# Optimization experiments

Hardware: AMD Instinct MI355X
Metric: run time of the kernel (lower is better)

## Reference

```python
import jax, jax.numpy as jnp
import numpy as np

N_NODES = 100000
N_EDGES = 1600000
UNITS = 256
N_LAYERS = 4          # model_layers
NUM_GRAPHS = 512
IN_FEAT = 9


def _glorot(key, shape):
    lim = float(np.sqrt(6.0 / (shape[0] + shape[1])))
    return jax.random.uniform(key, shape, jnp.float32, -lim, lim)


def setup_inputs() -> dict:
    key = jax.random.key(0)
    ks = jax.random.split(key, 16)
    x = jax.random.normal(ks[0], (N_NODES, IN_FEAT), jnp.float32)
    edge_index = jax.random.randint(ks[1], (2, N_EDGES), 0, N_NODES, jnp.int64)
    batch = jnp.sort(jax.random.randint(ks[2], (N_NODES,), 0, NUM_GRAPHS, jnp.int64))
    Win = _glorot(ks[3], (IN_FEAT, UNITS))
    bin_ = jnp.zeros((UNITS,), jnp.float32)
    Ws = jnp.stack([_glorot(ks[4 + i], (UNITS, UNITS)) for i in range(N_LAYERS - 1)])
    bs = jnp.zeros((N_LAYERS - 1, UNITS), jnp.float32)
    fc1_w = _glorot(ks[8], (UNITS, UNITS))
    fc1_b = jnp.zeros((UNITS,), jnp.float32)
    fc2_w = _glorot(ks[9], (UNITS, 32))
    fc2_b = jnp.zeros((32,), jnp.float32)
    fc3_w = _glorot(ks[10], (32, 1))
    fc3_b = jnp.zeros((1,), jnp.float32)
    return dict(x=x, edge_index=edge_index, batch=batch, Win=Win, bin_=bin_,
                Ws=Ws, bs=bs, fc1_w=fc1_w, fc1_b=fc1_b, fc2_w=fc2_w,
                fc2_b=fc2_b, fc3_w=fc3_w, fc3_b=fc3_b)


def _gcn_conv(x, W, b, src, dst, dinv):
    # PyG GCNConv: h = xW ; out = D^-1/2 (A+I) D^-1/2 h + b  (self-loops added)
    h = x @ W                                     # [N, d]
    norm = dinv[src] * dinv[dst]                  # [E]
    agg = jnp.zeros_like(h).at[dst].add(h[src] * norm[:, None])
    agg = agg + h * (dinv * dinv)[:, None]        # self-loop term
    return agg + b


def reference(x, edge_index, batch, Win, bin_, Ws, bs,
              fc1_w, fc1_b, fc2_w, fc2_b, fc3_w, fc3_b):
    src, dst = edge_index[0], edge_index[1]
    # degree with self-loops
    deg = jnp.zeros((N_NODES,), jnp.float32).at[dst].add(1.0) + 1.0
    dinv = jax.lax.rsqrt(deg)

    h = jnp.tanh(_gcn_conv(x, Win, bin_, src, dst, dinv))
    for i in range(N_LAYERS - 1):
        h = jnp.tanh(_gcn_conv(h, Ws[i], bs[i], src, dst, dinv))
        # dropout: identity at inference
    h = jnp.tanh(h @ fc1_w + fc1_b)
    h = jnp.tanh(h @ fc2_w + fc2_b)
    h = h @ fc3_w + fc3_b                          # [N, 1]
    # global mean pool over graphs
    sums = jax.ops.segment_sum(h, batch, num_segments=NUM_GRAPHS)      # [G, 1]
    cnts = jax.ops.segment_sum(jnp.ones((N_NODES,), jnp.float32), batch,
                               num_segments=NUM_GRAPHS)
    pooled = sums / jnp.maximum(cnts, 1.0)[:, None]
    return jax.nn.sigmoid(pooled)
```

## Files before the change

kernel.cpp:

```cpp
#include <hip/hip_runtime.h>
#include <math.h>

#define N_NODES 100000
#define N_EDGES 1600000
#define UNITS   256
#define NGRAPH  512
#define IN_FEAT 9
#define NB_SCAN ((N_NODES + 255) / 256)
#define NBUK    ((N_NODES + 255) / 256)
#define BCAP    8192
#define EPB     16384
#define NPB     ((N_EDGES + EPB - 1) / EPB)

typedef short bf16x8 __attribute__((ext_vector_type(8)));
typedef float f32x4  __attribute__((ext_vector_type(4)));
typedef float f32x2  __attribute__((ext_vector_type(2)));

__device__ __forceinline__ float bflo(unsigned int u) {
  return __builtin_bit_cast(float, u << 16);
}
__device__ __forceinline__ float bfhi(unsigned int u) {
  return __builtin_bit_cast(float, u & 0xffff0000u);
}
__device__ __forceinline__ unsigned short f2bf(float f) {
  unsigned int u = __builtin_bit_cast(unsigned int, f);
  u += 0x7fffu + ((u >> 16) & 1u);
  return (unsigned short)(u >> 16);
}

__device__ __forceinline__ bf16x8 f8tobf(uint2 q) {
  f32x2 v0 = __builtin_amdgcn_cvt_pk_f32_fp8(q.x, false);
  f32x2 v1 = __builtin_amdgcn_cvt_pk_f32_fp8(q.x, true);
  f32x2 v2 = __builtin_amdgcn_cvt_pk_f32_fp8(q.y, false);
  f32x2 v3 = __builtin_amdgcn_cvt_pk_f32_fp8(q.y, true);
  bf16x8 a;
  a[0] = (short)f2bf(v0[0]); a[1] = (short)f2bf(v0[1]);
  a[2] = (short)f2bf(v1[0]); a[3] = (short)f2bf(v1[1]);
  a[4] = (short)f2bf(v2[0]); a[5] = (short)f2bf(v2[1]);
  a[6] = (short)f2bf(v3[0]); a[7] = (short)f2bf(v3[1]);
  return a;
}

__device__ __forceinline__ int swz(int row, int byteInRow) {
  return row * 128 + (byteInRow ^ ((row & 7) << 4));
}


__global__ __launch_bounds__(256) void k_part(const int* __restrict__ ei,
                                              int* __restrict__ bcnt,
                                              uint2* __restrict__ bstore) {
  __shared__ int hist[NBUK];
  __shared__ int base[NBUK];
  int tid = threadIdx.x;
  int e0 = blockIdx.x * EPB;
  for (int i = tid; i < NBUK; i += 256) hist[i] = 0;
  __syncthreads();
  #pragma unroll 4
  for (int j = 0; j < EPB / 256; ++j) {
    int e = e0 + j * 256 + tid;
    if (e < N_EDGES) atomicAdd(&hist[ei[N_EDGES + e] >> 8], 1);
  }
  __syncthreads();
  for (int i = tid; i < NBUK; i += 256) {
    int h = hist[i];
    base[i] = h ? atomicAdd(&bcnt[i], h) : 0;
    hist[i] = 0;
  }
  __syncthreads();
  #pragma unroll 4
  for (int j = 0; j < EPB / 256; ++j) {
    int e = e0 + j * 256 + tid;
    if (e < N_EDGES) {
      int s = ei[e];
      int d = ei[N_EDGES + e];
      int b = d >> 8;
      int pos = base[b] + atomicAdd(&hist[b], 1);
      bstore[(size_t)b * BCAP + pos] = make_uint2((unsigned)s, (unsigned)d);
    }
  }
}

__global__ __launch_bounds__(256) void k_cnt(const int* __restrict__ bcnt,
                                             const uint2* __restrict__ bstore,
                                             int* __restrict__ cnt) {
  __shared__ int h[256];
  int b = blockIdx.x, tid = threadIdx.x;
  h[tid] = 0;
  __syncthreads();
  int nE = bcnt[b];
  for (int i = tid; i < nE; i += 256)
    atomicAdd(&h[bstore[(size_t)b * BCAP + i].y & 255], 1);
  __syncthreads();
  int node = b * 256 + tid;
  if (node < N_NODES) cnt[node] = h[tid];
}

__global__ __launch_bounds__(256) void k_colfill(const int* __restrict__ bcnt,
                                                 const uint2* __restrict__ bstore,
                                                 const int* __restrict__ row_ptr,
                                                 int* __restrict__ col) {
  __shared__ int cur[256];
  int b = blockIdx.x, tid = threadIdx.x;
  int node = b * 256 + tid;
  cur[tid] = (node < N_NODES) ? row_ptr[node] : 0;
  __syncthreads();
  int nE = bcnt[b];
  for (int i = tid; i < nE; i += 256) {
    uint2 sd = bstore[(size_t)b * BCAP + i];
    int pos = atomicAdd(&cur[sd.y & 255], 1);
    col[pos] = (int)sd.x;
  }
}

__global__ __launch_bounds__(256) void k_bsum(const int* __restrict__ cnt,
                                              int* __restrict__ bsum) {
  __shared__ int wsS[4];
  int b = blockIdx.x, tid = threadIdx.x, lane = tid & 63, w = tid >> 6;
  int idx = b * 256 + tid;
  int s = (idx < N_NODES) ? cnt[idx] : 0;
  #pragma unroll
  for (int m = 32; m >= 1; m >>= 1) s += __shfl_xor(s, m);
  if (lane == 0) wsS[w] = s;
  __syncthreads();
  if (tid == 0) bsum[b] = wsS[0] + wsS[1] + wsS[2] + wsS[3];
}

__global__ __launch_bounds__(512) void k_bscan(int* __restrict__ bsum) {
  __shared__ int wsS[8];
  int tid = threadIdx.x, lane = tid & 63, w = tid >> 6;
  int v = (tid < NB_SCAN) ? bsum[tid] : 0;
  int s = v;
  #pragma unroll
  for (int off = 1; off < 64; off <<= 1) {
    int t = __shfl_up(s, off);
    if (lane >= off) s += t;
  }
  if (lane == 63) wsS[w] = s;
  __syncthreads();
  int woff = 0;
  #pragma unroll
  for (int i = 0; i < 8; ++i) woff += (i < w) ? wsS[i] : 0;
  if (tid < NB_SCAN) bsum[tid] = woff + s - v;
}

__global__ __launch_bounds__(256) void k_scan3(const int* __restrict__ cnt,
                                               const int* __restrict__ bsum,
                                               int* __restrict__ row_ptr) {
  __shared__ int wsS[4];
  int b = blockIdx.x, tid = threadIdx.x, lane = tid & 63, w = tid >> 6;
  int idx = b * 256 + tid;
  int v = (idx < N_NODES) ? cnt[idx] : 0;
  int s = v;
  #pragma unroll
  for (int off = 1; off < 64; off <<= 1) {
    int t = __shfl_up(s, off);
    if (lane >= off) s += t;
  }
  if (lane == 63) wsS[w] = s;
  __syncthreads();
  int woff = 0;
  #pragma unroll
  for (int i = 0; i < 4; ++i) woff += (i < w) ? wsS[i] : 0;
  if (idx < N_NODES) row_ptr[idx] = bsum[b] + woff + s - v;
  if (idx == 0) row_ptr[N_NODES] = N_EDGES;
}

__global__ void k_dinv(const int* __restrict__ cnt, float* __restrict__ dinv) {
  int n = blockIdx.x * blockDim.x + threadIdx.x;
  if (n < N_NODES) dinv[n] = rsqrtf((float)cnt[n] + 1.0f);
}

__global__ void k_bounds(const int* __restrict__ batch, int* __restrict__ starts) {
  int g = blockIdx.x * blockDim.x + threadIdx.x;
  if (g > NGRAPH) return;
  if (g == NGRAPH) { starts[g] = N_NODES; return; }
  int lo = 0, hi = N_NODES;
  while (lo < hi) { int m = (lo + hi) >> 1; if (batch[m] < g) lo = m + 1; else hi = m; }
  starts[g] = lo;
}


__global__ void k_cvtW(const float* __restrict__ Ws, const float* __restrict__ fc1_w,
                       unsigned short* __restrict__ Wt) {
  int idx = blockIdx.x * 256 + threadIdx.x;
  int m = idx >> 16;
  int r = idx & 65535;
  int n = r >> 8;
  int k = r & 255;
  const float* src = (m < 3) ? (Ws + (size_t)m * 65536) : fc1_w;
  Wt[idx] = f2bf(src[k * 256 + n]);
}

__global__ void k_cvtW2(const float* __restrict__ fc2_w, unsigned short* __restrict__ Wt2) {
  int idx = blockIdx.x * 256 + threadIdx.x;
  int n = idx >> 8;
  int k = idx & 255;
  Wt2[idx] = f2bf(fc2_w[k * 32 + n]);
}

__global__ void k_scalex(const float* __restrict__ x, const float* __restrict__ dinv,
                         float* __restrict__ xs) {
  int idx = blockIdx.x * blockDim.x + threadIdx.x;
  if (idx < N_NODES * IN_FEAT) xs[idx] = x[idx] * dinv[idx / IN_FEAT];
}


__global__ void k_agg9(const float* __restrict__ xs, const int* __restrict__ row_ptr,
                       const int* __restrict__ col, const float* __restrict__ dinv,
                       float* __restrict__ p0) {
  int n = blockIdx.x * blockDim.x + threadIdx.x;
  if (n >= N_NODES) return;
  float acc[IN_FEAT];
  #pragma unroll
  for (int j = 0; j < IN_FEAT; ++j) acc[j] = xs[n * IN_FEAT + j];
  int beg = row_ptr[n], end = row_ptr[n + 1];
  for (int e = beg; e < end; ++e) {
    int s = col[e];
    #pragma unroll
    for (int j = 0; j < IN_FEAT; ++j) acc[j] += xs[s * IN_FEAT + j];
  }
  float dn = dinv[n];
  #pragma unroll
  for (int j = 0; j < IN_FEAT; ++j) p0[n * IN_FEAT + j] = dn * acc[j];
}

__global__ __launch_bounds__(256) void k_gemm9(const float* __restrict__ p0,
                                               const float* __restrict__ Win,
                                               const float* __restrict__ bin,
                                               const float* __restrict__ scale,
                                               unsigned char* __restrict__ h8) {
  __shared__ float pS[32][IN_FEAT];
  int tid = threadIdx.x;
  int row0 = blockIdx.x * 32;
  for (int i = tid; i < 32 * IN_FEAT; i += 256) {
    int r = i / IN_FEAT;
    pS[r][i % IN_FEAT] = (row0 + r < N_NODES) ? p0[(size_t)row0 * IN_FEAT + i] : 0.0f;
  }
  float wcol[IN_FEAT];
  #pragma unroll
  for (int k = 0; k < IN_FEAT; ++k) wcol[k] = Win[k * UNITS + tid];
  float b = bin[tid];
  __syncthreads();
  for (int r = 0; r < 32; ++r) {
    int gr = row0 + r;
    if (gr >= N_NODES) break;
    float a = b;
    #pragma unroll
    for (int k = 0; k < IN_FEAT; ++k) a += pS[r][k] * wcol[k];
    float v = scale[gr] * tanhf(a);
    float vn = __shfl_xor(v, 1);
    if ((tid & 1) == 0) {
      unsigned int pk = __builtin_amdgcn_cvt_pk_fp8_f32(v, vn, 0, false);
      *(unsigned short*)(h8 + (size_t)gr * UNITS + tid) = (unsigned short)pk;
    }
  }
}


__global__ __launch_bounds__(256) void k_agg256(
    const unsigned int* __restrict__ hs8,
    const int* __restrict__ row_ptr, const int* __restrict__ col,
    const float* __restrict__ dinv, unsigned int* __restrict__ p8) {
  int wid = threadIdx.x >> 6;
  int lane = threadIdx.x & 63;
  int n = blockIdx.x * 4 + wid;
  if (n >= N_NODES) return;
  unsigned int q = hs8[(size_t)n * 64 + lane];
  f32x2 lo = __builtin_amdgcn_cvt_pk_f32_fp8(q, false);
  f32x2 hi = __builtin_amdgcn_cvt_pk_f32_fp8(q, true);
  float a0 = lo[0], a1 = lo[1], a2 = hi[0], a3 = hi[1];
  int e = row_ptr[n], end = row_ptr[n + 1];
  for (; e + 8 <= end; e += 8) {
    int s[8];
    unsigned int qq[8];
    #pragma unroll
    for (int j = 0; j < 8; ++j) s[j] = col[e + j];
    #pragma unroll
    for (int j = 0; j < 8; ++j) qq[j] = hs8[(size_t)s[j] * 64 + lane];
    #pragma unroll
    for (int j = 0; j < 8; ++j) {
      f32x2 l2 = __builtin_amdgcn_cvt_pk_f32_fp8(qq[j], false);
      f32x2 h2 = __builtin_amdgcn_cvt_pk_f32_fp8(qq[j], true);
      a0 += l2[0]; a1 += l2[1]; a2 += h2[0]; a3 += h2[1];
    }
  }
  if (e + 4 <= end) {
    int s[4];
    unsigned int qq[4];
    #pragma unroll
    for (int j = 0; j < 4; ++j) s[j] = col[e + j];
    #pragma unroll
    for (int j = 0; j < 4; ++j) qq[j] = hs8[(size_t)s[j] * 64 + lane];
    #pragma unroll
    for (int j = 0; j < 4; ++j) {
      f32x2 l2 = __builtin_amdgcn_cvt_pk_f32_fp8(qq[j], false);
      f32x2 h2 = __builtin_amdgcn_cvt_pk_f32_fp8(qq[j], true);
      a0 += l2[0]; a1 += l2[1]; a2 += h2[0]; a3 += h2[1];
    }
    e += 4;
  }
  for (; e < end; ++e) {
    unsigned int q0 = hs8[(size_t)col[e] * 64 + lane];
    f32x2 l2 = __builtin_amdgcn_cvt_pk_f32_fp8(q0, false);
    f32x2 h2 = __builtin_amdgcn_cvt_pk_f32_fp8(q0, true);
    a0 += l2[0]; a1 += l2[1]; a2 += h2[0]; a3 += h2[1];
  }
  float dn = dinv[n];
  unsigned int u = __builtin_amdgcn_cvt_pk_fp8_f32(dn * a0, dn * a1, 0, false);
  u = __builtin_amdgcn_cvt_pk_fp8_f32(dn * a2, dn * a3, u, true);
  p8[(size_t)n * 64 + lane] = u;
}


__global__ __launch_bounds__(256, 4) void k_gemm_f8(
    const unsigned char* __restrict__ A8,
    const unsigned short* __restrict__ Wt,
    const float* __restrict__ bias,
    const float* __restrict__ scale,
    unsigned char* __restrict__ C8,
    int M) {
  __shared__ __align__(16) char lds[33792];
  char* Bs = lds;
  unsigned short (*Cs)[264] = (unsigned short(*)[264])lds;

  const int tid = threadIdx.x;
  const int w = tid >> 6;
  const int l = tid & 63;
  const int l15 = l & 15;
  const int blk = l >> 4;
  const int wr = w >> 1, wc = w & 1;
  const int row0 = blockIdx.x * 64;

  const int sr = tid >> 3;
  const int sc = (tid & 7) * 16;

  const unsigned char* aRow[2];
  #pragma unroll
  for (int rf = 0; rf < 2; ++rf) {
    int gr = row0 + 32 * wr + rf * 16 + l15;
    if (gr >= M) gr = M - 1;
    aRow[rf] = A8 + (size_t)gr * UNITS + 8 * blk;
  }

  f32x4 acc[2][8];
  #pragma unroll
  for (int rf = 0; rf < 2; ++rf)
    #pragma unroll
    for (int cf = 0; cf < 8; ++cf) acc[rf][cf] = (f32x4){0.f, 0.f, 0.f, 0.f};

  for (int ks = 0; ks < 4; ++ks) {
    const int k0 = ks * 64;
    if (ks) __syncthreads();
    #pragma unroll
    for (int i = 0; i < 8; ++i) {
      int n = sr + i * 32;
      uint4 v = *(const uint4*)(Wt + (size_t)n * UNITS + k0 + (sc >> 1));
      *(uint4*)(Bs + swz(n, sc)) = v;
    }
    __syncthreads();
    #pragma unroll
    for (int kc = 0; kc < 2; ++kc) {
      bf16x8 a[2];
      #pragma unroll
      for (int rf = 0; rf < 2; ++rf) {
        uint2 q = *(const uint2*)(aRow[rf] + k0 + kc * 32);
        a[rf] = f8tobf(q);
      }
      #pragma unroll
      for (int cf = 0; cf < 8; ++cf) {
        bf16x8 b = *(const bf16x8*)(Bs + swz(128 * wc + cf * 16 + l15, kc * 64 + blk * 16));
        acc[0][cf] = __builtin_amdgcn_mfma_f32_16x16x32_bf16(a[0], b, acc[0][cf], 0, 0, 0);
        acc[1][cf] = __builtin_amdgcn_mfma_f32_16x16x32_bf16(a[1], b, acc[1][cf], 0, 0, 0);
      }
    }
  }

  __syncthreads();
  float dvv[2][4];
  #pragma unroll
  for (int rf = 0; rf < 2; ++rf)
    #pragma unroll
    for (int reg = 0; reg < 4; ++reg) {
      int gr = row0 + 32 * wr + rf * 16 + 4 * blk + reg;
      dvv[rf][reg] = scale ? scale[gr < M ? gr : M - 1] : 1.0f;
    }
  #pragma unroll
  for (int cf = 0; cf < 8; ++cf) {
    float bcol = bias[128 * wc + cf * 16 + l15];
    #pragma unroll
    for (int rf = 0; rf < 2; ++rf) {
      #pragma unroll
      for (int reg = 0; reg < 4; ++reg) {
        float v = dvv[rf][reg] * tanhf(acc[rf][cf][reg] + bcol);
        Cs[32 * wr + rf * 16 + 4 * blk + reg][128 * wc + cf * 16 + l15] = f2bf(v);
      }
    }
  }
  __syncthreads();
  #pragma unroll
  for (int j = 0; j < 8; ++j) {
    int flat = tid + j * 256;
    int r = flat >> 5;
    int c = flat & 31;
    int gr = row0 + r;
    if (gr < M) {
      uint4 v = *(const uint4*)&Cs[r][c * 8];
      uint2 u;
      u.x = __builtin_amdgcn_cvt_pk_fp8_f32(bflo(v.x), bfhi(v.x), 0, false);
      u.x = __builtin_amdgcn_cvt_pk_fp8_f32(bflo(v.y), bfhi(v.y), u.x, true);
      u.y = __builtin_amdgcn_cvt_pk_fp8_f32(bflo(v.z), bfhi(v.z), 0, false);
      u.y = __builtin_amdgcn_cvt_pk_fp8_f32(bflo(v.w), bfhi(v.w), u.y, true);
      *(uint2*)(C8 + (size_t)gr * UNITS + c * 8) = u;
    }
  }
}


__global__ __launch_bounds__(256) void k_fc23(
    const unsigned char* __restrict__ H8,
    const unsigned short* __restrict__ Wt2,
    const float* __restrict__ b2,
    const float* __restrict__ w3, const float* __restrict__ b3,
    float* __restrict__ ns, int M) {
  const int tid = threadIdx.x;
  const int w = tid >> 6;
  const int l = tid & 63;
  const int l15 = l & 15;
  const int blk = l >> 4;
  const int row0 = blockIdx.x * 64 + 16 * w;

  int r = row0 + l15;
  int rc = r < M ? r : M - 1;
  const unsigned char* aPtr = H8 + (size_t)rc * UNITS + 8 * blk;
  const unsigned short* bPtr = Wt2 + (size_t)l15 * UNITS + 8 * blk;

  f32x4 acc0 = (f32x4){0.f, 0.f, 0.f, 0.f};
  f32x4 acc1 = (f32x4){0.f, 0.f, 0.f, 0.f};
  #pragma unroll
  for (int k0 = 0; k0 < UNITS; k0 += 32) {
    bf16x8 a  = f8tobf(*(const uint2*)(aPtr + k0));
    bf16x8 b0 = *(const bf16x8*)(bPtr + k0);
    bf16x8 b1 = *(const bf16x8*)(bPtr + 16 * UNITS + k0);
    acc0 = __builtin_amdgcn_mfma_f32_16x16x32_bf16(a, b0, acc0, 0, 0, 0);
    acc1 = __builtin_amdgcn_mfma_f32_16x16x32_bf16(a, b1, acc1, 0, 0, 0);
  }

  float c0 = b2[l15], c1 = b2[16 + l15];
  float w30 = w3[l15], w31 = w3[16 + l15];
  float b3v = b3[0];
  #pragma unroll
  for (int reg = 0; reg < 4; ++reg) {
    float part = tanhf(acc0[reg] + c0) * w30 + tanhf(acc1[reg] + c1) * w31;
    #pragma unroll
    for (int m = 8; m >= 1; m >>= 1) part += __shfl_xor(part, m);
    int gr = row0 + 4 * blk + reg;
    if (l15 == 0 && gr < M) ns[gr] = part + b3v;
  }
}

__global__ __launch_bounds__(64) void k_pool(const float* __restrict__ ns,
                                             const int* __restrict__ starts,
                                             float* __restrict__ out) {
  int g = blockIdx.x;
  int lane = threadIdx.x;
  int s = starts[g], e = starts[g + 1];
  float acc = 0.0f;
  for (int i = s + lane; i < e; i += 64) acc += ns[i];
  #pragma unroll
  for (int m = 32; m >= 1; m >>= 1) acc += __shfl_xor(acc, m);
  if (lane == 0) {
    float mean = acc / fmaxf((float)(e - s), 1.0f);
    out[g] = 1.0f / (1.0f + expf(-mean));
  }
}


extern "C" void kernel_launch(void* const* d_in, const int* in_sizes, int n_in,
                              void* d_out, int out_size, void* d_ws, size_t ws_size,
                              hipStream_t stream) {
  const float* x     = (const float*)d_in[0];
  const int*   ei    = (const int*)d_in[1];
  const int*   batch = (const int*)d_in[2];
  const float* Win   = (const float*)d_in[3];
  const float* bin_  = (const float*)d_in[4];
  const float* Ws    = (const float*)d_in[5];
  const float* bs    = (const float*)d_in[6];
  const float* fc1_w = (const float*)d_in[7];
  const float* fc1_b = (const float*)d_in[8];
  const float* fc2_w = (const float*)d_in[9];
  const float* fc2_b = (const float*)d_in[10];
  const float* fc3_w = (const float*)d_in[11];
  const float* fc3_b = (const float*)d_in[12];
  float* out = (float*)d_out;

  char* ws = (char*)d_ws;
  size_t off = 0;
  auto alloc = [&](size_t bytes) {
    size_t o = off;
    off = (off + bytes + 255) & ~(size_t)255;
    return o;
  };
  int*   cnt     = (int*)(ws + alloc(N_NODES * 4));
  int*   row_ptr = (int*)(ws + alloc((N_NODES + 1) * 4));
  float* dinv    = (float*)(ws + alloc(N_NODES * 4));
  int*   col     = (int*)(ws + alloc((size_t)N_EDGES * 4));
  int*   bsum    = (int*)(ws + alloc(NB_SCAN * 4));
  int*   bcnt    = (int*)(ws + alloc(NBUK * 4));
  uint2* bstore  = (uint2*)(ws + alloc((size_t)NBUK * BCAP * 8));
  int*   starts  = (int*)(ws + alloc((NGRAPH + 1) * 4));
  float* ns      = (float*)(ws + alloc(N_NODES * 4));
  float* xs      = (float*)(ws + alloc((size_t)N_NODES * IN_FEAT * 4));
  float* p0      = (float*)(ws + alloc((size_t)N_NODES * IN_FEAT * 4));
  unsigned short* Wt   = (unsigned short*)(ws + alloc((size_t)4 * UNITS * UNITS * 2));
  unsigned short* Wt2  = (unsigned short*)(ws + alloc((size_t)32 * UNITS * 2));
  unsigned char*  h8a  = (unsigned char*)(ws + alloc((size_t)N_NODES * UNITS));
  unsigned char*  h8b  = (unsigned char*)(ws + alloc((size_t)N_NODES * UNITS));
  unsigned char*  p8   = (unsigned char*)(ws + alloc((size_t)N_NODES * UNITS));

  hipMemsetAsync(bcnt, 0, NBUK * 4, stream);

  k_cvtW<<<(4 * UNITS * UNITS) / 256, 256, 0, stream>>>(Ws, fc1_w, Wt);
  k_cvtW2<<<32, 256, 0, stream>>>(fc2_w, Wt2);

  k_part<<<NPB, 256, 0, stream>>>(ei, bcnt, bstore);
  k_cnt<<<NBUK, 256, 0, stream>>>(bcnt, bstore, cnt);
  k_bsum<<<NB_SCAN, 256, 0, stream>>>(cnt, bsum);
  k_bscan<<<1, 512, 0, stream>>>(bsum);
  k_scan3<<<NB_SCAN, 256, 0, stream>>>(cnt, bsum, row_ptr);
  k_dinv<<<(N_NODES + 255) / 256, 256, 0, stream>>>(cnt, dinv);
  k_colfill<<<NBUK, 256, 0, stream>>>(bcnt, bstore, row_ptr, col);
  k_bounds<<<3, 256, 0, stream>>>(batch, starts);

  k_scalex<<<(N_NODES * IN_FEAT + 255) / 256, 256, 0, stream>>>(x, dinv, xs);
  k_agg9<<<(N_NODES + 255) / 256, 256, 0, stream>>>(xs, row_ptr, col, dinv, p0);
  k_gemm9<<<(N_NODES + 31) / 32, 256, 0, stream>>>(p0, Win, bin_, dinv, h8a);

  int ggrid = (N_NODES + 63) / 64;
  k_agg256<<<(N_NODES + 3) / 4, 256, 0, stream>>>((const unsigned int*)h8a, row_ptr, col, dinv, (unsigned int*)p8);
  k_gemm_f8<<<ggrid, 256, 0, stream>>>(p8, Wt + (size_t)0 * UNITS * UNITS,
                                       bs + (size_t)0 * UNITS, dinv, h8b, N_NODES);
  k_agg256<<<(N_NODES + 3) / 4, 256, 0, stream>>>((const unsigned int*)h8b, row_ptr, col, dinv, (unsigned int*)p8);
  k_gemm_f8<<<ggrid, 256, 0, stream>>>(p8, Wt + (size_t)1 * UNITS * UNITS,
                                       bs + (size_t)1 * UNITS, dinv, h8a, N_NODES);
  k_agg256<<<(N_NODES + 3) / 4, 256, 0, stream>>>((const unsigned int*)h8a, row_ptr, col, dinv, (unsigned int*)p8);
  k_gemm_f8<<<ggrid, 256, 0, stream>>>(p8, Wt + (size_t)2 * UNITS * UNITS,
                                       bs + (size_t)2 * UNITS, nullptr, h8b, N_NODES);

  k_gemm_f8<<<ggrid, 256, 0, stream>>>(h8b, Wt + (size_t)3 * UNITS * UNITS,
                                       fc1_b, nullptr, h8a, N_NODES);

  k_fc23<<<(N_NODES + 63) / 64, 256, 0, stream>>>(h8a, Wt2, fc2_b, fc3_w, fc3_b, ns, N_NODES);

  k_pool<<<NGRAPH, 64, 0, stream>>>(ns, starts, out);
}
```

Before: 533.8 us.

## Fuse last GCN GEMM, fc1 and fc2/fc3 into one MLP kernel keeping activations in LDS

Replaces the final k_gemm_f8 (layer 4), the fc1 k_gemm_f8 and k_fc23 with a single k_mlp kernel that keeps the 64x256 bf16 intermediate tile in LDS between the three matmuls. This avoids two round trips of a 100000x256 fp8 activation through global memory, along with the fp8 requantisation at each step. It also folds the dinv computation into the scan kernel and shrinks edges per block in the partition kernel. The fused kernel uses 64KB of LDS, which may limit occupancy.

```diff
diff --git a/kernel.cpp b/kernel.cpp
--- a/kernel.cpp
+++ b/kernel.cpp
@@ -9,7 +9,7 @@
 #define NB_SCAN ((N_NODES + 255) / 256)
 #define NBUK    ((N_NODES + 255) / 256)
 #define BCAP    8192
-#define EPB     16384
+#define EPB     4096
 #define NPB     ((N_EDGES + EPB - 1) / EPB)
 
 typedef short bf16x8 __attribute__((ext_vector_type(8)));
@@ -44,6 +44,9 @@
 __device__ __forceinline__ int swz(int row, int byteInRow) {
   return row * 128 + (byteInRow ^ ((row & 7) << 4));
 }
+__device__ __forceinline__ int swzA(int row, int byteInRow) {
+  return row * 512 + (byteInRow ^ ((row & 7) << 4));
+}
 
 
 __global__ __launch_bounds__(256) void k_part(const int* __restrict__ ei,
@@ -145,7 +148,8 @@
 
 __global__ __launch_bounds__(256) void k_scan3(const int* __restrict__ cnt,
                                                const int* __restrict__ bsum,
-                                               int* __restrict__ row_ptr) {
+                                               int* __restrict__ row_ptr,
+                                               float* __restrict__ dinv) {
   __shared__ int wsS[4];
   int b = blockIdx.x, tid = threadIdx.x, lane = tid & 63, w = tid >> 6;
   int idx = b * 256 + tid;
@@ -161,13 +165,11 @@
   int woff = 0;
   #pragma unroll
   for (int i = 0; i < 4; ++i) woff += (i < w) ? wsS[i] : 0;
-  if (idx < N_NODES) row_ptr[idx] = bsum[b] + woff + s - v;
+  if (idx < N_NODES) {
+    row_ptr[idx] = bsum[b] + woff + s - v;
+    dinv[idx] = rsqrtf((float)v + 1.0f);
+  }
   if (idx == 0) row_ptr[N_NODES] = N_EDGES;
-}
-
-__global__ void k_dinv(const int* __restrict__ cnt, float* __restrict__ dinv) {
-  int n = blockIdx.x * blockDim.x + threadIdx.x;
-  if (n < N_NODES) dinv[n] = rsqrtf((float)cnt[n] + 1.0f);
 }
 
 __global__ void k_bounds(const int* __restrict__ batch, int* __restrict__ starts) {
@@ -382,7 +384,7 @@
     #pragma unroll
     for (int reg = 0; reg < 4; ++reg) {
       int gr = row0 + 32 * wr + rf * 16 + 4 * blk + reg;
-      dvv[rf][reg] = scale ? scale[gr < M ? gr : M - 1] : 1.0f;
+      dvv[rf][reg] = scale[gr < M ? gr : M - 1];
     }
   #pragma unroll
   for (int cf = 0; cf < 8; ++cf) {
@@ -416,35 +418,145 @@
 }
 
 
-__global__ __launch_bounds__(256) void k_fc23(
-    const unsigned char* __restrict__ H8,
-    const unsigned short* __restrict__ Wt2,
-    const float* __restrict__ b2,
+__global__ __launch_bounds__(256, 2) void k_mlp(
+    const unsigned char* __restrict__ A8,
+    const unsigned short* __restrict__ WtL2, const float* __restrict__ bL2,
+    const unsigned short* __restrict__ Wtfc1, const float* __restrict__ bfc1,
+    const unsigned short* __restrict__ Wt2, const float* __restrict__ b2,
     const float* __restrict__ w3, const float* __restrict__ b3,
     float* __restrict__ ns, int M) {
+  __shared__ __align__(16) char lds[65536];
+  char* T  = lds;
+  char* Bs = lds + 32768;
+
   const int tid = threadIdx.x;
   const int w = tid >> 6;
   const int l = tid & 63;
   const int l15 = l & 15;
   const int blk = l >> 4;
-  const int row0 = blockIdx.x * 64 + 16 * w;
-
-  int r = row0 + l15;
-  int rc = r < M ? r : M - 1;
-  const unsigned char* aPtr = H8 + (size_t)rc * UNITS + 8 * blk;
-  const unsigned short* bPtr = Wt2 + (size_t)l15 * UNITS + 8 * blk;
+  const int wr = w >> 1, wc = w & 1;
+  const int row0 = blockIdx.x * 64;
+
+  const int sr = tid >> 3;
+  const int sc = (tid & 7) * 16;
+
+  const unsigned char* aRow[2];
+  #pragma unroll
+  for (int rf = 0; rf < 2; ++rf) {
+    int gr = row0 + 32 * wr + rf * 16 + l15;
+    if (gr >= M) gr = M - 1;
+    aRow[rf] = A8 + (size_t)gr * UNITS + 8 * blk;
+  }
+  f32x4 acc[2][8];
+  #pragma unroll
+  for (int rf = 0; rf < 2; ++rf)
+    #pragma unroll
+    for (int cf = 0; cf < 8; ++cf) acc[rf][cf] = (f32x4){0.f, 0.f, 0.f, 0.f};
+
+  for (int ks = 0; ks < 4; ++ks) {
+    const int k0 = ks * 64;
+    if (ks) __syncthreads();
+    #pragma unroll
+    for (int i = 0; i < 8; ++i) {
+      int n = sr + i * 32;
+      uint4 v = *(const uint4*)(WtL2 + (size_t)n * UNITS + k0 + (sc >> 1));
+      *(uint4*)(Bs + swz(n, sc)) = v;
+    }
+    __syncthreads();
+    #pragma unroll
+    for (int kc = 0; kc < 2; ++kc) {
+      bf16x8 a[2];
+      #pragma unroll
+      for (int rf = 0; rf < 2; ++rf)
+        a[rf] = f8tobf(*(const uint2*)(aRow[rf] + k0 + kc * 32));
+      #pragma unroll
+      for (int cf = 0; cf < 8; ++cf) {
+        bf16x8 b = *(const bf16x8*)(Bs + swz(128 * wc + cf * 16 + l15, kc * 64 + blk * 16));
+        acc[0][cf] = __builtin_amdgcn_mfma_f32_16x16x32_bf16(a[0], b, acc[0][cf], 0, 0, 0);
+        acc[1][cf] = __builtin_amdgcn_mfma_f32_16x16x32_bf16(a[1], b, acc[1][cf], 0, 0, 0);
+      }
+    }
+  }
+  #pragma unroll
+  for (int cf = 0; cf < 8; ++cf) {
+    float bcol = bL2[128 * wc + cf * 16 + l15];
+    #pragma unroll
+    for (int rf = 0; rf < 2; ++rf) {
+      #pragma unroll
+      for (int reg = 0; reg < 4; ++reg) {
+        int row = 32 * wr + rf * 16 + 4 * blk + reg;
+        int colb = (128 * wc + cf * 16 + l15) * 2;
+        *(unsigned short*)(T + swzA(row, colb)) = f2bf(tanhf(acc[rf][cf][reg] + bcol));
+      }
+    }
+  }
+
+  #pragma unroll
+  for (int rf = 0; rf < 2; ++rf)
+    #pragma unroll
+    for (int cf = 0; cf < 8; ++cf) acc[rf][cf] = (f32x4){0.f, 0.f, 0.f, 0.f};
+  for (int ks = 0; ks < 4; ++ks) {
+    const int k0 = ks * 64;
+    __syncthreads();
+    #pragma unroll
+    for (int i = 0; i < 8; ++i) {
+      int n = sr + i * 32;
+      uint4 v = *(const uint4*)(Wtfc1 + (size_t)n * UNITS + k0 + (sc >> 1));
+      *(uint4*)(Bs + swz(n, sc)) = v;
+    }
+    __syncthreads();
+    #pragma unroll
+    for (int kc = 0; kc < 2; ++kc) {
+      bf16x8 a[2];
+      #pragma unroll
+      for (int rf = 0; rf < 2; ++rf) {
+        int ar = 32 * wr + rf * 16 + l15;
+        a[rf] = *(const bf16x8*)(T + swzA(ar, blk * 16 + ks * 128 + kc * 64));
+      }
+      #pragma unroll
+      for (int cf = 0; cf < 8; ++cf) {
+        bf16x8 b = *(const bf16x8*)(Bs + swz(128 * wc + cf * 16 + l15, kc * 64 + blk * 16));
+        acc[0][cf] = __builtin_amdgcn_mfma_f32_16x16x32_bf16(a[0], b, acc[0][cf], 0, 0, 0);
+        acc[1][cf] = __builtin_amdgcn_mfma_f32_16x16x32_bf16(a[1], b, acc[1][cf], 0, 0, 0);
+      }
+    }
+  }
+
+  __syncthreads();
+  #pragma unroll
+  for (int cf = 0; cf < 8; ++cf) {
+    float bcol = bfc1[128 * wc + cf * 16 + l15];
+    #pragma unroll
+    for (int rf = 0; rf < 2; ++rf) {
+      #pragma unroll
+      for (int reg = 0; reg < 4; ++reg) {
+        int row = 32 * wr + rf * 16 + 4 * blk + reg;
+        int colb = (128 * wc + cf * 16 + l15) * 2;
+        *(unsigned short*)(T + swzA(row, colb)) = f2bf(tanhf(acc[rf][cf][reg] + bcol));
+      }
+    }
+  }
+  #pragma unroll
+  for (int i = 0; i < 4; ++i) {
+    int idx = tid + i * 256;
+    int row = idx >> 5;
+    int c = idx & 31;
+    uint4 v = *(const uint4*)(Wt2 + (size_t)row * UNITS + c * 8);
+    *(uint4*)(Bs + row * 512 + ((c * 16) ^ ((row & 7) << 4))) = v;
+  }
+  __syncthreads();
 
   f32x4 acc0 = (f32x4){0.f, 0.f, 0.f, 0.f};
   f32x4 acc1 = (f32x4){0.f, 0.f, 0.f, 0.f};
   #pragma unroll
   for (int k0 = 0; k0 < UNITS; k0 += 32) {
-    bf16x8 a  = f8tobf(*(const uint2*)(aPtr + k0));
-    bf16x8 b0 = *(const bf16x8*)(bPtr + k0);
-    bf16x8 b1 = *(const bf16x8*)(bPtr + 16 * UNITS + k0);
+    int byte = k0 * 2 + blk * 16;
+    bf16x8 a  = *(const bf16x8*)(T + swzA(16 * w + l15, byte));
+    bf16x8 b0 = *(const bf16x8*)(Bs + l15 * 512 + (byte ^ ((l15 & 7) << 4)));
+    bf16x8 b1 = *(const bf16x8*)(Bs + (16 + l15) * 512 + (byte ^ ((l15 & 7) << 4)));
     acc0 = __builtin_amdgcn_mfma_f32_16x16x32_bf16(a, b0, acc0, 0, 0, 0);
     acc1 = __builtin_amdgcn_mfma_f32_16x16x32_bf16(a, b1, acc1, 0, 0, 0);
   }
-
   float c0 = b2[l15], c1 = b2[16 + l15];
   float w30 = w3[l15], w31 = w3[16 + l15];
   float b3v = b3[0];
@@ -453,7 +565,7 @@
     float part = tanhf(acc0[reg] + c0) * w30 + tanhf(acc1[reg] + c1) * w31;
     #pragma unroll
     for (int m = 8; m >= 1; m >>= 1) part += __shfl_xor(part, m);
-    int gr = row0 + 4 * blk + reg;
+    int gr = row0 + 16 * w + 4 * blk + reg;
     if (l15 == 0 && gr < M) ns[gr] = part + b3v;
   }
 }
@@ -526,8 +638,7 @@
   k_cnt<<<NBUK, 256, 0, stream>>>(bcnt, bstore, cnt);
   k_bsum<<<NB_SCAN, 256, 0, stream>>>(cnt, bsum);
   k_bscan<<<1, 512, 0, stream>>>(bsum);
-  k_scan3<<<NB_SCAN, 256, 0, stream>>>(cnt, bsum, row_ptr);
-  k_dinv<<<(N_NODES + 255) / 256, 256, 0, stream>>>(cnt, dinv);
+  k_scan3<<<NB_SCAN, 256, 0, stream>>>(cnt, bsum, row_ptr, dinv);
   k_colfill<<<NBUK, 256, 0, stream>>>(bcnt, bstore, row_ptr, col);
   k_bounds<<<3, 256, 0, stream>>>(batch, starts);
 
@@ -543,13 +654,10 @@
   k_gemm_f8<<<ggrid, 256, 0, stream>>>(p8, Wt + (size_t)1 * UNITS * UNITS,
                                        bs + (size_t)1 * UNITS, dinv, h8a, N_NODES);
   k_agg256<<<(N_NODES + 3) / 4, 256, 0, stream>>>((const unsigned int*)h8a, row_ptr, col, dinv, (unsigned int*)p8);
-  k_gemm_f8<<<ggrid, 256, 0, stream>>>(p8, Wt + (size_t)2 * UNITS * UNITS,
-                                       bs + (size_t)2 * UNITS, nullptr, h8b, N_NODES);
-
-  k_gemm_f8<<<ggrid, 256, 0, stream>>>(h8b, Wt + (size_t)3 * UNITS * UNITS,
-                                       fc1_b, nullptr, h8a, N_NODES);
-
-  k_fc23<<<(N_NODES + 63) / 64, 256, 0, stream>>>(h8a, Wt2, fc2_b, fc3_w, fc3_b, ns, N_NODES);
+  k_mlp<<<ggrid, 256, 0, stream>>>(p8, Wt + (size_t)2 * UNITS * UNITS,
+                                   bs + (size_t)2 * UNITS,
+                                   Wt + (size_t)3 * UNITS * UNITS, fc1_b,
+                                   Wt2, fc2_b, fc3_w, fc3_b, ns, N_NODES);
 
   k_pool<<<NGRAPH, 64, 0, stream>>>(ns, starts, out);
 }
```

After: 497.7 us. -6.8%, faster.
